# Kernel optimization log

Hardware: AMD Instinct MI355X
Metric: run time of the kernel (lower is better)

Reference implementation:

```python
import jax, jax.numpy as jnp
import numpy as np

HID = 512
VOCAB = 2048
K_CB = 4


def conv1d(x, w, b, stride):
    # x: [B, C_in, L], w: [C_out, C_in, 7], torch Conv1d(k=7, stride, pad=3)
    y = jax.lax.conv_general_dilated(
        x, w, window_strides=(stride,), padding=[(3, 3)],
        dimension_numbers=("NCH", "OIH", "NCH"))
    return y + b[None, :, None]


def setup_inputs() -> dict:
    key = jax.random.key(0)
    ks = jax.random.split(key, 9)
    B, S = 4, 32768
    audio = jax.random.normal(ks[0], (B, 1, S), dtype=jnp.float32)
    # encoder params (fan-in scaled init, like torch default scale-wise)
    w1 = jax.random.normal(ks[1], (HID // 4, 1, 7), dtype=jnp.float32) * (1.0 / np.sqrt(1 * 7))
    b1 = jnp.zeros((HID // 4,), dtype=jnp.float32)
    w2 = jax.random.normal(ks[2], (HID // 2, HID // 4, 7), dtype=jnp.float32) * (1.0 / np.sqrt(HID // 4 * 7))
    b2 = jnp.zeros((HID // 2,), dtype=jnp.float32)
    w3 = jax.random.normal(ks[3], (HID, HID // 2, 7), dtype=jnp.float32) * (1.0 / np.sqrt(HID // 2 * 7))
    b3 = jnp.zeros((HID,), dtype=jnp.float32)
    codebook = jax.random.normal(ks[4], (K_CB, VOCAB, HID), dtype=jnp.float32)
    embedding = jax.random.normal(ks[5], (VOCAB, HID), dtype=jnp.float32)
    return {"audio": audio, "w1": w1, "b1": b1, "w2": w2, "b2": b2,
            "w3": w3, "b3": b3, "codebook": codebook, "embedding": embedding}


def reference(audio, w1, b1, w2, b2, w3, b3, codebook, embedding):
    # conv encoder: [B,1,S] -> [B,H,L], L = S/8
    f = jax.nn.relu(conv1d(audio, w1, b1, 2))
    f = jax.nn.relu(conv1d(f, w2, b2, 2))
    f = conv1d(f, w3, b3, 2)
    feats = jnp.transpose(f, (0, 2, 1))  # [B, L, H]

    # multi-codebook nearest neighbor: argmin of squared L2 == argmin of cdist
    f2 = jnp.sum(feats * feats, axis=-1)          # [B, L]
    c2 = jnp.sum(codebook * codebook, axis=-1)    # [K, V]
    cross = jnp.einsum("blh,kvh->bklv", feats, codebook)  # [B, K, L, V]
    d2 = f2[:, None, :, None] + c2[None, :, None, :] - 2.0 * cross
    tokens = jnp.argmin(d2, axis=-1)              # [B, K, L] (stack over codebooks at dim=1)
    emb = embedding[tokens].mean(axis=1)          # [B, L, H]
    return tokens, emb
```

## Files before the change

kernel.cpp:

```cpp
#include <hip/hip_runtime.h>
#include <hip/hip_bf16.h>
#include <stdint.h>

#define B_ 4
#define S_IN 32768
#define C1V 128
#define L1V 16384
#define C2V 256
#define L2V 8192
#define C3V 512
#define L3V 4096
#define VOCABV 2048
#define KCB 4

typedef _Float16 half8 __attribute__((ext_vector_type(8)));
typedef float floatx4 __attribute__((ext_vector_type(4)));

#define AS1 __attribute__((address_space(1)))
#define AS3 __attribute__((address_space(3)))

__device__ __forceinline__ void gload_lds16(const void* g, void* l) {
    __builtin_amdgcn_global_load_lds((const AS1 void*)g, (AS3 void*)l, 16, 0, 0);
}

__device__ __forceinline__ half8 lds_read_half8_a4(const _Float16* p) {
    union { uint32_t u[4]; half8 h; } t;
    const uint32_t* w = (const uint32_t*)p;
    t.u[0] = w[0]; t.u[1] = w[1]; t.u[2] = w[2]; t.u[3] = w[3];
    return t.h;
}

__global__ void conv1_kernel(const float* __restrict__ x, const float* __restrict__ w,
                             const float* __restrict__ bias, float* __restrict__ out) {
    __shared__ float xs[2 * 256 + 6];
    __shared__ float ws[7];
    const int l0 = blockIdx.x * 256;
    const int co = blockIdx.y;
    const int b  = blockIdx.z;
    const int tid = threadIdx.x;
    const float* xb = x + (size_t)b * S_IN;
    for (int n = tid; n < 2 * 256 + 6; n += 256) {
        int p = 2 * l0 - 3 + n;
        xs[n] = (p >= 0 && p < S_IN) ? xb[p] : 0.f;
    }
    if (tid < 7) ws[tid] = w[co * 7 + tid];
    __syncthreads();
    float acc = bias[co];
    const int base = 2 * tid;
#pragma unroll
    for (int t = 0; t < 7; ++t) acc = fmaf(ws[t], xs[base + t], acc);
    acc = fmaxf(acc, 0.f);
    out[((size_t)(b * C1V + co)) * L1V + l0 + tid] = acc;
}

__global__ void wsplit_kernel(const float* __restrict__ w, _Float16* __restrict__ wh,
                              _Float16* __restrict__ wl, int cin, int cout) {
    int idx = blockIdx.x * 256 + threadIdx.x;
    if (idx >= cin * cout) return;
    int co = idx / cin;
    int ci = idx - co * cin;
    const float* src = w + ((size_t)co * cin + ci) * 7;
    half8 h, l;
    h[0] = (_Float16)0.f; l[0] = (_Float16)0.f;
#pragma unroll
    for (int u = 1; u < 8; ++u) {
        float v = src[u - 1] * 1024.f;
        _Float16 hh = (_Float16)v;
        h[u] = hh;
        l[u] = (_Float16)(v - (float)hh);
    }
    size_t o = (size_t)co * (cin * 8) + ci * 8;
    *(half8*)(wh + o) = h;
    *(half8*)(wl + o) = l;
}

__global__ __launch_bounds__(256, 2) void conv2_mfma_kernel(
    const float* __restrict__ in, const _Float16* __restrict__ WH,
    const _Float16* __restrict__ WL, const float* __restrict__ bias,
    float* __restrict__ out) {
    __shared__ _Float16 XsH[4 * 272], XsL[4 * 272];
    __shared__ _Float16 WsH[128 * 32], WsL[128 * 32];
    const int tid = threadIdx.x;
    const int wave = tid >> 6;
    const int lane = tid & 63;
    const int wm = wave >> 1, wn = wave & 1;
    const int q  = lane >> 4;
    const int cl = lane & 15;
    const int l0  = blockIdx.x * 128;
    const int co0 = blockIdx.y * 128;
    const int b   = blockIdx.z;
    const float* inb = in + (size_t)b * C1V * L1V;

    const int wrow  = lane >> 2;
    const int wseg  = lane & 3;
    const int wsoff = (wseg ^ ((wrow >> 1) & 3)) * 8;
    const int rq    = (q ^ ((cl >> 1) & 3)) * 8;

    floatx4 acc[4][4];
#pragma unroll
    for (int a = 0; a < 4; ++a)
#pragma unroll
        for (int n = 0; n < 4; ++n) acc[a][n] = (floatx4){0.f, 0.f, 0.f, 0.f};

    for (int ch = 0; ch < 32; ++ch) {
        __syncthreads();
        for (int n = tid; n < 4 * 264; n += 256) {
            int ci = n / 264;
            int m  = n - ci * 264;
            int p  = 2 * l0 - 4 + m;
            float v = (p >= 0 && p < L1V) ? inb[(size_t)(ch * 4 + ci) * L1V + p] * 1024.f : 0.f;
            _Float16 h = (_Float16)v;
            XsH[ci * 272 + m] = h;
            XsL[ci * 272 + m] = (_Float16)(v - (float)h);
        }
        const int k0 = ch * 32;
        for (int g = wave; g < 8; g += 4) {
            const _Float16* gh = WH + (size_t)(co0 + g * 16 + wrow) * 1024 + k0 + wsoff;
            const _Float16* gl = WL + (size_t)(co0 + g * 16 + wrow) * 1024 + k0 + wsoff;
            gload_lds16(gh, (char*)WsH + g * 1024);
            gload_lds16(gl, (char*)WsL + g * 1024);
        }
        asm volatile("s_waitcnt vmcnt(0)" ::: "memory");
        __syncthreads();

        half8 awh[4], awl[4], bxh[4], bxl[4];
#pragma unroll
        for (int a = 0; a < 4; ++a) {
            const int ro = (wm * 64 + a * 16 + cl) * 32 + rq;
            awh[a] = *(const half8*)&WsH[ro];
            awl[a] = *(const half8*)&WsL[ro];
        }
#pragma unroll
        for (int n = 0; n < 4; ++n) {
            const int lrel = wn * 64 + n * 16 + cl;
            bxh[n] = lds_read_half8_a4(&XsH[q * 272 + 2 * lrel]);
            bxl[n] = lds_read_half8_a4(&XsL[q * 272 + 2 * lrel]);
        }
#pragma unroll
        for (int a = 0; a < 4; ++a)
#pragma unroll
            for (int n = 0; n < 4; ++n) {
                acc[a][n] = __builtin_amdgcn_mfma_f32_16x16x32_f16(awh[a], bxh[n], acc[a][n], 0, 0, 0);
                acc[a][n] = __builtin_amdgcn_mfma_f32_16x16x32_f16(awl[a], bxh[n], acc[a][n], 0, 0, 0);
                acc[a][n] = __builtin_amdgcn_mfma_f32_16x16x32_f16(awh[a], bxl[n], acc[a][n], 0, 0, 0);
            }
    }

    float bv[4][4];
#pragma unroll
    for (int a = 0; a < 4; ++a)
#pragma unroll
        for (int r = 0; r < 4; ++r) bv[a][r] = bias[co0 + wm * 64 + a * 16 + q * 4 + r];
#pragma unroll
    for (int a = 0; a < 4; ++a)
#pragma unroll
        for (int n = 0; n < 4; ++n) {
            const int l = l0 + wn * 64 + n * 16 + cl;
#pragma unroll
            for (int r = 0; r < 4; ++r) {
                const int co = co0 + wm * 64 + a * 16 + q * 4 + r;
                float vv = fmaxf(acc[a][n][r] * (1.f / 1048576.f) + bv[a][r], 0.f);
                out[((size_t)(b * C2V + co)) * L2V + l] = vv;
            }
        }
}

__global__ __launch_bounds__(256, 2) void conv3_mfma_kernel(
    const float* __restrict__ in, const _Float16* __restrict__ WH,
    const _Float16* __restrict__ WL, const float* __restrict__ bias,
    _Float16* __restrict__ outh) {
    __shared__ _Float16 XsH[4 * 272], XsL[4 * 272];
    __shared__ _Float16 WsH[128 * 32], WsL[128 * 32];
    const int tid = threadIdx.x;
    const int wave = tid >> 6;
    const int lane = tid & 63;
    const int wm = wave >> 1, wn = wave & 1;
    const int q  = lane >> 4;
    const int cl = lane & 15;
    const int l0  = blockIdx.x * 128;
    const int co0 = blockIdx.y * 128;
    const int b   = blockIdx.z;
    const float* inb = in + (size_t)b * C2V * L2V;

    const int wrow  = lane >> 2;
    const int wseg  = lane & 3;
    const int wsoff = (wseg ^ ((wrow >> 1) & 3)) * 8;
    const int rq    = (q ^ ((cl >> 1) & 3)) * 8;

    floatx4 acc[4][4];
#pragma unroll
    for (int a = 0; a < 4; ++a)
#pragma unroll
        for (int n = 0; n < 4; ++n) acc[a][n] = (floatx4){0.f, 0.f, 0.f, 0.f};

    for (int ch = 0; ch < 64; ++ch) {
        __syncthreads();
        for (int n = tid; n < 4 * 264; n += 256) {
            int ci = n / 264;
            int m  = n - ci * 264;
            int p  = 2 * l0 - 4 + m;
            float v = (p >= 0 && p < L2V) ? inb[(size_t)(ch * 4 + ci) * L2V + p] * 1024.f : 0.f;
            _Float16 h = (_Float16)v;
            XsH[ci * 272 + m] = h;
            XsL[ci * 272 + m] = (_Float16)(v - (float)h);
        }
        const int k0 = ch * 32;
        for (int g = wave; g < 8; g += 4) {
            const _Float16* gh = WH + (size_t)(co0 + g * 16 + wrow) * 2048 + k0 + wsoff;
            const _Float16* gl = WL + (size_t)(co0 + g * 16 + wrow) * 2048 + k0 + wsoff;
            gload_lds16(gh, (char*)WsH + g * 1024);
            gload_lds16(gl, (char*)WsL + g * 1024);
        }
        asm volatile("s_waitcnt vmcnt(0)" ::: "memory");
        __syncthreads();

        half8 axh[4], axl[4], bwh[4], bwl[4];
#pragma unroll
        for (int a = 0; a < 4; ++a) {
            const int lrel = wm * 64 + a * 16 + cl;
            axh[a] = lds_read_half8_a4(&XsH[q * 272 + 2 * lrel]);
            axl[a] = lds_read_half8_a4(&XsL[q * 272 + 2 * lrel]);
        }
#pragma unroll
        for (int n = 0; n < 4; ++n) {
            const int ro = (wn * 64 + n * 16 + cl) * 32 + rq;
            bwh[n] = *(const half8*)&WsH[ro];
            bwl[n] = *(const half8*)&WsL[ro];
        }
#pragma unroll
        for (int a = 0; a < 4; ++a)
#pragma unroll
            for (int n = 0; n < 4; ++n) {
                acc[a][n] = __builtin_amdgcn_mfma_f32_16x16x32_f16(axh[a], bwh[n], acc[a][n], 0, 0, 0);
                acc[a][n] = __builtin_amdgcn_mfma_f32_16x16x32_f16(axl[a], bwh[n], acc[a][n], 0, 0, 0);
                acc[a][n] = __builtin_amdgcn_mfma_f32_16x16x32_f16(axh[a], bwl[n], acc[a][n], 0, 0, 0);
            }
    }

    float bv[4];
#pragma unroll
    for (int n = 0; n < 4; ++n) bv[n] = bias[co0 + wn * 64 + n * 16 + cl];
#pragma unroll
    for (int a = 0; a < 4; ++a)
#pragma unroll
        for (int n = 0; n < 4; ++n) {
            const int co = co0 + wn * 64 + n * 16 + cl;
#pragma unroll
            for (int r = 0; r < 4; ++r) {
                const int l = l0 + wm * 64 + a * 16 + q * 4 + r;
                float f = acc[a][n][r] * (1.f / 1048576.f) + bv[n];
                float s = f * 1024.f;
                _Float16 h = (_Float16)s;
                _Float16 lo = (_Float16)(s - (float)h);
                _Float16* dst = outh + ((size_t)b * L3V + l) * 1024 + co;
                dst[0] = h;
                dst[512] = lo;
            }
        }
}

__global__ void cbprep_kernel(const float* __restrict__ cb, _Float16* __restrict__ y,
                              float* __restrict__ c2p) {
    const int r = blockIdx.x;
    const int lane = threadIdx.x;
    const float* row = cb + (size_t)r * 512;
    float4 a = *(const float4*)&row[lane * 8];
    float4 c = *(const float4*)&row[lane * 8 + 4];
    float s = a.x * a.x + a.y * a.y + a.z * a.z + a.w * a.w
            + c.x * c.x + c.y * c.y + c.z * c.z + c.w * c.w;
#pragma unroll
    for (int off = 32; off > 0; off >>= 1) s += __shfl_down(s, off, 64);
    if (lane == 0) c2p[r] = s * 524288.f;

    const float e[8] = {a.x, a.y, a.z, a.w, c.x, c.y, c.z, c.w};
    half8 hv, lv;
#pragma unroll
    for (int i = 0; i < 8; ++i) {
        float v = e[i] * 1024.f;
        _Float16 h = (_Float16)v;
        hv[i] = h;
        lv[i] = (_Float16)(v - (float)h);
    }
    *(half8*)(y + (size_t)r * 1024 + lane * 8) = hv;
    *(half8*)(y + (size_t)r * 1024 + 512 + lane * 8) = lv;
}

__global__ __launch_bounds__(512, 2) void cross_mfma_kernel(
    const _Float16* __restrict__ Af, const _Float16* __restrict__ Bf,
    const float* __restrict__ c2p,
    int* __restrict__ tok_i, float* __restrict__ tok_f) {

    __shared__ _Float16 AsH[2][8192], AsL[2][8192];
    __shared__ _Float16 BsH[2][8192], BsL[2][8192];
    __shared__ float c2s[2048];
    __shared__ float slotv[2][256];
    __shared__ int   sloti[2][256];

    const int tid  = threadIdx.x;
    const int w    = tid >> 6;
    const int lane = tid & 63;
    const int wm = w >> 1;
    const int wn = w & 1;
    const int q  = lane >> 4;
    const int cl = lane & 15;

    const int l0 = blockIdx.x * 256;
    const int k  = blockIdx.y;
    const int b  = blockIdx.z;

    const _Float16* Ab = Af + (size_t)(b * L3V + l0) * 1024;
    const _Float16* Bb = Bf + (size_t)k * VOCABV * 1024;

    {
        float4 cv = *(const float4*)&c2p[k * VOCABV + tid * 4];
        *(float4*)&c2s[tid * 4] = cv;
    }
    if (tid < 256) {
        slotv[0][tid] = -3.4e38f; slotv[1][tid] = -3.4e38f;
        sloti[0][tid] = 0;        sloti[1][tid] = 0;
    }

    const int arow  = w * 16 + (lane >> 2);
    const int bg    = (w >> 1) & 1;
    const int bj    = (w & 1) * 16 + (lane >> 2);
    const int bpl   = w >> 2;
    const int sswz8 = ((lane & 3) ^ ((lane >> 3) & 3)) * 8;
    const int brq   = (q ^ ((cl >> 1) & 3)) * 8;

#define STAGE_A(NXT, KON, PL, H) do { \
    const _Float16* s_ = Ab + (size_t)((H) * 128 + arow) * 1024 + (PL) * 512 + (KON) + sswz8; \
    gload_lds16(s_, ((PL) ? (char*)&AsL[NXT][0] : (char*)&AsH[NXT][0]) \
                     + (H) * 8192 + w * 1024 + lane * 16); \
} while (0)
#define STAGE_B(NXT, VTN, KON, C) do { \
    const _Float16* s_ = Bb + (size_t)((VTN) * 256 + 128 * bg + 32 * (C) + bj) * 1024 \
                         + bpl * 512 + (KON) + sswz8; \
    gload_lds16(s_, (bpl ? (char*)&BsL[NXT][0] : (char*)&BsH[NXT][0]) \
                     + (C) * 4096 + (w & 3) * 1024 + lane * 16); \
} while (0)

    floatx4 acc[4][8];
    half8 ah[4], al[4];
    int cur = 0;

    STAGE_A(0, 0, 0, 0); STAGE_A(0, 0, 0, 1);
    STAGE_A(0, 0, 1, 0); STAGE_A(0, 0, 1, 1);
    STAGE_B(0, 0, 0, 0); STAGE_B(0, 0, 0, 1);
    STAGE_B(0, 0, 0, 2); STAGE_B(0, 0, 0, 3);

#define PHASE(P, VMC) do { \
    asm volatile("s_waitcnt vmcnt(" #VMC ")" ::: "memory"); \
    __builtin_amdgcn_s_barrier(); \
    if ((P) == 0) { \
        _Pragma("unroll") \
        for (int mt = 0; mt < 4; ++mt) { \
            const int aro = (wm * 64 + mt * 16 + cl) * 32 + brq; \
            ah[mt] = *(const half8*)&AsH[cur][aro]; \
            al[mt] = *(const half8*)&AsL[cur][aro]; \
        } \
    } \
    const int bro0_ = (P) * 2048 + wn * 1024 + cl * 32 + brq; \
    const int bro1_ = bro0_ + 512; \
    half8 bh0_ = *(const half8*)&BsH[cur][bro0_]; \
    half8 bl0_ = *(const half8*)&BsL[cur][bro0_]; \
    half8 bh1_ = *(const half8*)&BsH[cur][bro1_]; \
    half8 bl1_ = *(const half8*)&BsL[cur][bro1_]; \
    if ((P) == 0)      { STAGE_A(nxt, kon, 0, 0); STAGE_A(nxt, kon, 0, 1); } \
    else if ((P) == 1) { STAGE_A(nxt, kon, 1, 0); STAGE_A(nxt, kon, 1, 1); } \
    else if ((P) == 2) { STAGE_B(nxt, vtn, kon, 0); STAGE_B(nxt, vtn, kon, 1); } \
    else               { STAGE_B(nxt, vtn, kon, 2); STAGE_B(nxt, vtn, kon, 3); } \
    asm volatile("s_waitcnt lgkmcnt(0)" ::: "memory"); \
    __builtin_amdgcn_sched_barrier(0); \
    __builtin_amdgcn_s_setprio(1); \
    _Pragma("unroll") \
    for (int mt = 0; mt < 4; ++mt) { \
        acc[mt][2*(P)]   = __builtin_amdgcn_mfma_f32_16x16x32_f16(ah[mt], bh0_, acc[mt][2*(P)], 0, 0, 0); \
        acc[mt][2*(P)]   = __builtin_amdgcn_mfma_f32_16x16x32_f16(al[mt], bh0_, acc[mt][2*(P)], 0, 0, 0); \
        acc[mt][2*(P)]   = __builtin_amdgcn_mfma_f32_16x16x32_f16(ah[mt], bl0_, acc[mt][2*(P)], 0, 0, 0); \
        acc[mt][2*(P)+1] = __builtin_amdgcn_mfma_f32_16x16x32_f16(ah[mt], bh1_, acc[mt][2*(P)+1], 0, 0, 0); \
        acc[mt][2*(P)+1] = __builtin_amdgcn_mfma_f32_16x16x32_f16(al[mt], bh1_, acc[mt][2*(P)+1], 0, 0, 0); \
        acc[mt][2*(P)+1] = __builtin_amdgcn_mfma_f32_16x16x32_f16(ah[mt], bl1_, acc[mt][2*(P)+1], 0, 0, 0); \
    } \
    __builtin_amdgcn_s_setprio(0); \
    __builtin_amdgcn_sched_barrier(0); \
} while (0)

#pragma unroll 1
    for (int t = 0; t < 128; ++t) {
        const int nxt = cur ^ 1;
        const int tn  = t + 1;
        const int vtn = tn >> 4;
        const int kon = (tn & 15) << 5;
        const int vt  = t >> 4;

        if ((t & 15) == 0) {
#pragma unroll
            for (int mt = 0; mt < 4; ++mt)
#pragma unroll
                for (int nt = 0; nt < 8; ++nt) acc[mt][nt] = (floatx4){0.f, 0.f, 0.f, 0.f};
        }

        { PHASE(0, 3); }
        { PHASE(1, 4); }
        { PHASE(2, 5); }
        { PHASE(3, 6); }
        cur = nxt;

        if ((t & 15) == 15) {
            float c2v[8];
#pragma unroll
            for (int nt = 0; nt < 8; ++nt)
                c2v[nt] = c2s[vt * 256 + wn * 128 + nt * 16 + cl];
#pragma unroll
            for (int mt = 0; mt < 4; ++mt)
#pragma unroll
                for (int r = 0; r < 4; ++r) {
                    float bv = acc[mt][0][r] - c2v[0];
                    int   bi = vt * 256 + wn * 128 + cl;
#pragma unroll
                    for (int nt = 1; nt < 8; ++nt) {
                        float m = acc[mt][nt][r] - c2v[nt];
                        int   vi = vt * 256 + wn * 128 + nt * 16 + cl;
                        if (m > bv) { bv = m; bi = vi; }
                    }
#pragma unroll
                    for (int msk = 1; msk < 16; msk <<= 1) {
                        float ov = __shfl_xor(bv, msk, 64);
                        int   oi = __shfl_xor(bi, msk, 64);
                        if (ov > bv || (ov == bv && oi < bi)) { bv = ov; bi = oi; }
                    }
                    if (cl == 0) {
                        const int row = wm * 64 + mt * 16 + q * 4 + r;
                        float cur_v = slotv[wn][row];
                        int   ci  = sloti[wn][row];
                        if (bv > cur_v || (bv == cur_v && bi < ci)) {
                            slotv[wn][row] = bv;
                            sloti[wn][row] = bi;
                        }
                    }
                }
        }
    }
#undef PHASE
#undef STAGE_A
#undef STAGE_B

    __syncthreads();
    if (tid < 256) {
        float v0 = slotv[0][tid], v1 = slotv[1][tid];
        int   i0 = sloti[0][tid], i1 = sloti[1][tid];
        bool t1 = (v1 > v0);
        int best = t1 ? i1 : i0;
        const int n = (b * KCB + k) * L3V + l0 + tid;
        tok_i[n] = best;
        tok_f[n] = (float)best;
    }
}

__global__ void emb_kernel(const int* __restrict__ tokens, const float* __restrict__ E,
                           float* __restrict__ out) {
    const int l = blockIdx.x;
    const int b = blockIdx.y;
    const int h4 = threadIdx.x * 4;
    const int t0 = tokens[((size_t)(b * KCB + 0)) * L3V + l];
    const int t1 = tokens[((size_t)(b * KCB + 1)) * L3V + l];
    const int t2 = tokens[((size_t)(b * KCB + 2)) * L3V + l];
    const int t3 = tokens[((size_t)(b * KCB + 3)) * L3V + l];
    const float4 e0 = *(const float4*)&E[(size_t)t0 * 512 + h4];
    const float4 e1 = *(const float4*)&E[(size_t)t1 * 512 + h4];
    const float4 e2 = *(const float4*)&E[(size_t)t2 * 512 + h4];
    const float4 e3 = *(const float4*)&E[(size_t)t3 * 512 + h4];
    float4 r;
    r.x = (e0.x + e1.x + e2.x + e3.x) * 0.25f;
    r.y = (e0.y + e1.y + e2.y + e3.y) * 0.25f;
    r.z = (e0.z + e1.z + e2.z + e3.z) * 0.25f;
    r.w = (e0.w + e1.w + e2.w + e3.w) * 0.25f;
    *(float4*)&out[((size_t)b * L3V + l) * 512 + h4] = r;
}

extern "C" void kernel_launch(void* const* d_in, const int* in_sizes, int n_in,
                              void* d_out, int out_size, void* d_ws, size_t ws_size,
                              hipStream_t stream) {
    const float* audio = (const float*)d_in[0];
    const float* w1 = (const float*)d_in[1];
    const float* b1 = (const float*)d_in[2];
    const float* w2 = (const float*)d_in[3];
    const float* b2 = (const float*)d_in[4];
    const float* w3 = (const float*)d_in[5];
    const float* b3 = (const float*)d_in[6];
    const float* cb = (const float*)d_in[7];
    const float* E  = (const float*)d_in[8];

    float* out_tok = (float*)d_out;
    float* out_emb = out_tok + (size_t)B_ * KCB * L3V;

    float* ws = (float*)d_ws;
    size_t off = 0;
    float* x1  = ws + off; off += (size_t)B_ * C1V * L1V;
    float* x2f = ws + off; off += (size_t)B_ * C2V * L2V / 2;
    float* bfh_f = ws + off; off += (size_t)KCB * VOCABV * 1024 / 2;
    float* w2h_f = ws + off; off += (size_t)C2V * (C1V * 8) / 2;
    float* w2l_f = ws + off; off += (size_t)C2V * (C1V * 8) / 2;
    float* w3h_f = ws + off; off += (size_t)C3V * (C2V * 8) / 2;
    float* w3l_f = ws + off; off += (size_t)C3V * (C2V * 8) / 2;
    float* c2p = ws + off; off += (size_t)KCB * VOCABV;
    int*   tok = (int*)(ws + off); off += (size_t)B_ * KCB * L3V;

    _Float16* Afh = (_Float16*)x1;
    _Float16* Bfh = (_Float16*)bfh_f;
    _Float16* W2H = (_Float16*)w2h_f; _Float16* W2L = (_Float16*)w2l_f;
    _Float16* W3H = (_Float16*)w3h_f; _Float16* W3L = (_Float16*)w3l_f;

    wsplit_kernel<<<(C2V * C1V + 255) / 256, 256, 0, stream>>>(w2, W2H, W2L, C1V, C2V);
    wsplit_kernel<<<(C3V * C2V + 255) / 256, 256, 0, stream>>>(w3, W3H, W3L, C2V, C3V);

    conv1_kernel<<<dim3(L1V / 256, C1V, B_), 256, 0, stream>>>(audio, w1, b1, x1);

    conv2_mfma_kernel<<<dim3(L2V / 128, C2V / 128, B_), 256, 0, stream>>>(
        x1, W2H, W2L, b2, x2f);

    conv3_mfma_kernel<<<dim3(L3V / 128, C3V / 128, B_), 256, 0, stream>>>(
        x2f, W3H, W3L, b3, Afh);

    cbprep_kernel<<<KCB * VOCABV, 64, 0, stream>>>(cb, Bfh, c2p);

    cross_mfma_kernel<<<dim3(L3V / 256, KCB, B_), 512, 0, stream>>>(
        Afh, Bfh, c2p, tok, out_tok);

    emb_kernel<<<dim3(L3V, B_), 128, 0, stream>>>(tok, E, out_emb);
}
```

Measured before the change: 734.9 us.

## Store conv activations as padded fp16 hi/lo planes and DMA them into LDS

```diff
diff --git a/kernel.cpp b/kernel.cpp
--- a/kernel.cpp
+++ b/kernel.cpp
@@ -13,6 +13,11 @@
 #define VOCABV 2048
 #define KCB 4
 
+#define R1P (2 * (L1V + 16))
+#define P1P (L1V + 16)
+#define R2P (2 * (L2V + 16))
+#define P2P (L2V + 16)
+
 typedef _Float16 half8 __attribute__((ext_vector_type(8)));
 typedef float floatx4 __attribute__((ext_vector_type(4)));
 
@@ -30,8 +35,25 @@
     return t.h;
 }
 
+__global__ void padzero_kernel(_Float16* __restrict__ x1h, _Float16* __restrict__ x2h) {
+    int j = blockIdx.x * 256 + threadIdx.x;
+    half8 z;
+#pragma unroll
+    for (int i = 0; i < 8; ++i) z[i] = (_Float16)0.f;
+    if (j < 2048) {
+        int row = j >> 2, p = j & 3;
+        size_t base = (size_t)row * R1P + (size_t)(p >> 1) * P1P + ((p & 1) ? (L1V + 8) : 0);
+        *(half8*)(x1h + base) = z;
+    } else if (j < 6144) {
+        int j2 = j - 2048;
+        int row = j2 >> 2, p = j2 & 3;
+        size_t base = (size_t)row * R2P + (size_t)(p >> 1) * P2P + ((p & 1) ? (L2V + 8) : 0);
+        *(half8*)(x2h + base) = z;
+    }
+}
+
 __global__ void conv1_kernel(const float* __restrict__ x, const float* __restrict__ w,
-                             const float* __restrict__ bias, float* __restrict__ out) {
+                             const float* __restrict__ bias, _Float16* __restrict__ out) {
     __shared__ float xs[2 * 256 + 6];
     __shared__ float ws[7];
     const int l0 = blockIdx.x * 256;
@@ -49,8 +71,12 @@
     const int base = 2 * tid;
 #pragma unroll
     for (int t = 0; t < 7; ++t) acc = fmaf(ws[t], xs[base + t], acc);
-    acc = fmaxf(acc, 0.f);
-    out[((size_t)(b * C1V + co)) * L1V + l0 + tid] = acc;
+    float s = fmaxf(acc, 0.f) * 1024.f;
+    _Float16 h  = (_Float16)s;
+    _Float16 lo = (_Float16)(s - (float)h);
+    size_t o = (size_t)(b * C1V + co) * R1P + 8 + l0 + tid;
+    out[o] = h;
+    out[o + P1P] = lo;
 }
 
 __global__ void wsplit_kernel(const float* __restrict__ w, _Float16* __restrict__ wh,
@@ -74,11 +100,12 @@
     *(half8*)(wl + o) = l;
 }
 
+
 __global__ __launch_bounds__(256, 2) void conv2_mfma_kernel(
-    const float* __restrict__ in, const _Float16* __restrict__ WH,
+    const _Float16* __restrict__ xin, const _Float16* __restrict__ WH,
     const _Float16* __restrict__ WL, const float* __restrict__ bias,
-    float* __restrict__ out) {
-    __shared__ _Float16 XsH[4 * 272], XsL[4 * 272];
+    _Float16* __restrict__ xout) {
+    __shared__ _Float16 Xs[2176];
     __shared__ _Float16 WsH[128 * 32], WsL[128 * 32];
     const int tid = threadIdx.x;
     const int wave = tid >> 6;
@@ -89,13 +116,18 @@
     const int l0  = blockIdx.x * 128;
     const int co0 = blockIdx.y * 128;
     const int b   = blockIdx.z;
-    const float* inb = in + (size_t)b * C1V * L1V;
 
     const int wrow  = lane >> 2;
     const int wseg  = lane & 3;
     const int wsoff = (wseg ^ ((wrow >> 1) & 3)) * 8;
     const int rq    = (q ^ ((cl >> 1) & 3)) * 8;
 
+    const int pl0 = (tid >= 136) ? 1 : 0;
+    const int r0  = tid - pl0 * 136;
+    const int ci0 = r0 / 34;
+    const int sg0 = r0 - ci0 * 34;
+    const _Float16* xb = xin + (size_t)b * C1V * R1P;
+
     floatx4 acc[4][4];
 #pragma unroll
     for (int a = 0; a < 4; ++a)
@@ -104,14 +136,13 @@
 
     for (int ch = 0; ch < 32; ++ch) {
         __syncthreads();
-        for (int n = tid; n < 4 * 264; n += 256) {
-            int ci = n / 264;
-            int m  = n - ci * 264;
-            int p  = 2 * l0 - 4 + m;
-            float v = (p >= 0 && p < L1V) ? inb[(size_t)(ch * 4 + ci) * L1V + p] * 1024.f : 0.f;
-            _Float16 h = (_Float16)v;
-            XsH[ci * 272 + m] = h;
-            XsL[ci * 272 + m] = (_Float16)(v - (float)h);
+        {
+            const _Float16* gx = xb + (size_t)(ch * 4 + ci0) * R1P + pl0 * P1P + 2 * l0 + sg0 * 8;
+            gload_lds16(gx, (char*)Xs + (tid & ~63) * 16);
+            if (tid < 16) {
+                const _Float16* gt = xb + (size_t)(ch * 4 + 3) * R1P + P1P + 2 * l0 + (18 + tid) * 8;
+                gload_lds16(gt, (char*)Xs + 4096);
+            }
         }
         const int k0 = ch * 32;
         for (int g = wave; g < 8; g += 4) {
@@ -133,8 +164,8 @@
 #pragma unroll
         for (int n = 0; n < 4; ++n) {
             const int lrel = wn * 64 + n * 16 + cl;
-            bxh[n] = lds_read_half8_a4(&XsH[q * 272 + 2 * lrel]);
-            bxl[n] = lds_read_half8_a4(&XsL[q * 272 + 2 * lrel]);
+            bxh[n] = lds_read_half8_a4(&Xs[q * 272 + 4 + 2 * lrel]);
+            bxl[n] = lds_read_half8_a4(&Xs[1088 + q * 272 + 4 + 2 * lrel]);
         }
 #pragma unroll
         for (int a = 0; a < 4; ++a)
@@ -160,16 +191,21 @@
             for (int r = 0; r < 4; ++r) {
                 const int co = co0 + wm * 64 + a * 16 + q * 4 + r;
                 float vv = fmaxf(acc[a][n][r] * (1.f / 1048576.f) + bv[a][r], 0.f);
-                out[((size_t)(b * C2V + co)) * L2V + l] = vv;
+                float s = vv * 1024.f;
+                _Float16 h  = (_Float16)s;
+                _Float16 lo = (_Float16)(s - (float)h);
+                size_t o = (size_t)(b * C2V + co) * R2P + 8 + l;
+                xout[o] = h;
+                xout[o + P2P] = lo;
             }
         }
 }
 
 __global__ __launch_bounds__(256, 2) void conv3_mfma_kernel(
-    const float* __restrict__ in, const _Float16* __restrict__ WH,
+    const _Float16* __restrict__ xin, const _Float16* __restrict__ WH,
     const _Float16* __restrict__ WL, const float* __restrict__ bias,
     _Float16* __restrict__ outh) {
-    __shared__ _Float16 XsH[4 * 272], XsL[4 * 272];
+    __shared__ _Float16 Xs[2176];
     __shared__ _Float16 WsH[128 * 32], WsL[128 * 32];
     const int tid = threadIdx.x;
     const int wave = tid >> 6;
@@ -180,13 +216,18 @@
     const int l0  = blockIdx.x * 128;
     const int co0 = blockIdx.y * 128;
     const int b   = blockIdx.z;
-    const float* inb = in + (size_t)b * C2V * L2V;
 
     const int wrow  = lane >> 2;
     const int wseg  = lane & 3;
     const int wsoff = (wseg ^ ((wrow >> 1) & 3)) * 8;
     const int rq    = (q ^ ((cl >> 1) & 3)) * 8;
 
+    const int pl0 = (tid >= 136) ? 1 : 0;
+    const int r0  = tid - pl0 * 136;
+    const int ci0 = r0 / 34;
+    const int sg0 = r0 - ci0 * 34;
+    const _Float16* xb = xin + (size_t)b * C2V * R2P;
+
     floatx4 acc[4][4];
 #pragma unroll
     for (int a = 0; a < 4; ++a)
@@ -195,14 +236,13 @@
 
     for (int ch = 0; ch < 64; ++ch) {
         __syncthreads();
-        for (int n = tid; n < 4 * 264; n += 256) {
-            int ci = n / 264;
-            int m  = n - ci * 264;
-            int p  = 2 * l0 - 4 + m;
-            float v = (p >= 0 && p < L2V) ? inb[(size_t)(ch * 4 + ci) * L2V + p] * 1024.f : 0.f;
-            _Float16 h = (_Float16)v;
-            XsH[ci * 272 + m] = h;
-            XsL[ci * 272 + m] = (_Float16)(v - (float)h);
+        {
+            const _Float16* gx = xb + (size_t)(ch * 4 + ci0) * R2P + pl0 * P2P + 2 * l0 + sg0 * 8;
+            gload_lds16(gx, (char*)Xs + (tid & ~63) * 16);
+            if (tid < 16) {
+                const _Float16* gt = xb + (size_t)(ch * 4 + 3) * R2P + P2P + 2 * l0 + (18 + tid) * 8;
+                gload_lds16(gt, (char*)Xs + 4096);
+            }
         }
         const int k0 = ch * 32;
         for (int g = wave; g < 8; g += 4) {
@@ -218,8 +258,8 @@
 #pragma unroll
         for (int a = 0; a < 4; ++a) {
             const int lrel = wm * 64 + a * 16 + cl;
-            axh[a] = lds_read_half8_a4(&XsH[q * 272 + 2 * lrel]);
-            axl[a] = lds_read_half8_a4(&XsL[q * 272 + 2 * lrel]);
+            axh[a] = lds_read_half8_a4(&Xs[q * 272 + 4 + 2 * lrel]);
+            axl[a] = lds_read_half8_a4(&Xs[1088 + q * 272 + 4 + 2 * lrel]);
         }
 #pragma unroll
         for (int n = 0; n < 4; ++n) {
@@ -496,9 +536,8 @@
 
     float* ws = (float*)d_ws;
     size_t off = 0;
-    float* x1  = ws + off; off += (size_t)B_ * C1V * L1V;
-    float* x2f = ws + off; off += (size_t)B_ * C2V * L2V / 2;
-    float* bfh_f = ws + off; off += (size_t)KCB * VOCABV * 1024 / 2;
+    float* x1f = ws + off; off += (size_t)B_ * C1V * (L1V + 16);
+    float* x2f = ws + off; off += (size_t)B_ * C2V * (L2V + 16);
     float* w2h_f = ws + off; off += (size_t)C2V * (C1V * 8) / 2;
     float* w2l_f = ws + off; off += (size_t)C2V * (C1V * 8) / 2;
     float* w3h_f = ws + off; off += (size_t)C3V * (C2V * 8) / 2;
@@ -506,21 +545,25 @@
     float* c2p = ws + off; off += (size_t)KCB * VOCABV;
     int*   tok = (int*)(ws + off); off += (size_t)B_ * KCB * L3V;
 
-    _Float16* Afh = (_Float16*)x1;
-    _Float16* Bfh = (_Float16*)bfh_f;
+    _Float16* X1  = (_Float16*)x1f;
+    _Float16* X2  = (_Float16*)x2f;
+    _Float16* Afh = (_Float16*)x1f;
+    _Float16* Bfh = (_Float16*)x2f;
     _Float16* W2H = (_Float16*)w2h_f; _Float16* W2L = (_Float16*)w2l_f;
     _Float16* W3H = (_Float16*)w3h_f; _Float16* W3L = (_Float16*)w3l_f;
 
+    padzero_kernel<<<24, 256, 0, stream>>>(X1, X2);
+
     wsplit_kernel<<<(C2V * C1V + 255) / 256, 256, 0, stream>>>(w2, W2H, W2L, C1V, C2V);
     wsplit_kernel<<<(C3V * C2V + 255) / 256, 256, 0, stream>>>(w3, W3H, W3L, C2V, C3V);
 
-    conv1_kernel<<<dim3(L1V / 256, C1V, B_), 256, 0, stream>>>(audio, w1, b1, x1);
+    conv1_kernel<<<dim3(L1V / 256, C1V, B_), 256, 0, stream>>>(audio, w1, b1, X1);
 
     conv2_mfma_kernel<<<dim3(L2V / 128, C2V / 128, B_), 256, 0, stream>>>(
-        x1, W2H, W2L, b2, x2f);
+        X1, W2H, W2L, b2, X2);
 
     conv3_mfma_kernel<<<dim3(L3V / 128, C3V / 128, B_), 256, 0, stream>>>(
-        x2f, W3H, W3L, b3, Afh);
+        X2, W3H, W3L, b3, Afh);
 
     cbprep_kernel<<<KCB * VOCABV, 64, 0, stream>>>(cb, Bfh, c2p);
 
```

New measurement: 595.7 us. 1.23x faster.
